# Optimization experiments

Measured on AMD Instinct MI355X. Metric: run time of the kernel, lower is better.

Reference implementation:

```python
import jax, jax.numpy as jnp
import numpy as np

C = 96
H = 4 * C  # hidden_channels = int(mlp_ratio * in_channels)
EPS = 1e-5  # torch LayerNorm default eps


def setup_inputs() -> dict:
    key = jax.random.key(0)
    ks = jax.random.split(key, 8)
    x = jax.random.normal(ks[0], (2, C, 64, 64, 64), dtype=jnp.float32)
    # depthwise conv3d: groups=C -> kernel (O=C, I/groups=1, 7,7,7)
    dw_w = jax.random.normal(ks[1], (C, 1, 7, 7, 7), dtype=jnp.float32) * 0.05
    dw_b = jax.random.normal(ks[2], (C,), dtype=jnp.float32) * 0.01
    ln_g = jnp.ones((C,), dtype=jnp.float32)
    ln_b = jnp.zeros((C,), dtype=jnp.float32)
    w1 = jax.random.normal(ks[3], (C, H), dtype=jnp.float32) * (1.0 / np.sqrt(C))
    b1 = jnp.zeros((H,), dtype=jnp.float32)
    w2 = jax.random.normal(ks[4], (H, C), dtype=jnp.float32) * (1.0 / np.sqrt(H))
    b2 = jnp.zeros((C,), dtype=jnp.float32)
    gamma = jnp.full((C,), 1e-6, dtype=jnp.float32)  # layer_scale init
    return {"x": x, "dw_w": dw_w, "dw_b": dw_b, "ln_g": ln_g, "ln_b": ln_b,
            "w1": w1, "b1": b1, "w2": w2, "b2": b2, "gamma": gamma}


def reference(x, dw_w, dw_b, ln_g, ln_b, w1, b1, w2, b2, gamma):
    # depthwise 3D conv, kernel 7, padding 3 (same), groups=C
    out = jax.lax.conv_general_dilated(
        x, dw_w, window_strides=(1, 1, 1), padding=[(3, 3)] * 3,
        dimension_numbers=("NCDHW", "OIDHW", "NCDHW"),
        feature_group_count=C)
    out = out + dw_b[None, :, None, None, None]
    # b c d h w -> b d h w c
    out = jnp.moveaxis(out, 1, -1)
    # LayerNorm over channel dim
    mu = jnp.mean(out, axis=-1, keepdims=True)
    var = jnp.mean(jnp.square(out - mu), axis=-1, keepdims=True)
    out = (out - mu) * jax.lax.rsqrt(var + EPS) * ln_g + ln_b
    # 2-layer MLP (pointwise convs as Linear), exact GELU like torch default
    out = jax.nn.gelu(out @ w1 + b1, approximate=False)
    out = out @ w2 + b2
    # layer scale
    out = gamma * out
    # b d h w c -> b c d h w, stochastic depth is identity (p=0), residual
    out = jnp.moveaxis(out, -1, 1)
    return out + x
```

## Files before the change

kernel.cpp:

```cpp
#include <hip/hip_runtime.h>

typedef unsigned int u32;
typedef unsigned short u16;
typedef unsigned long long u64;
typedef long i64;
typedef float f32x4 __attribute__((ext_vector_type(4)));
typedef float f32x2 __attribute__((ext_vector_type(2)));
typedef u32 u32x4 __attribute__((ext_vector_type(4)));

__device__ __forceinline__ u16 f2bf_rne(float f) {
    return __builtin_bit_cast(u16, (__bf16)f);
}
__device__ __forceinline__ float bf2f(u16 h) {
    return __builtin_bit_cast(float, ((u32)h) << 16);
}
__device__ __forceinline__ float gelu_fast(float v) {
    float t = __builtin_amdgcn_exp2f(v * -2.4554673f);
    return v * __builtin_amdgcn_rcpf(1.f + t);
}
__device__ __forceinline__ i64 mk64(u32 lo, u32 hi) {
    return (i64)(((u64)hi << 32) | (u64)lo);
}
__device__ __forceinline__ u32 pk4(float a, float b, float c, float d) {
    u32 w = (u32)__builtin_amdgcn_cvt_pk_fp8_f32(a, b, 0, false);
    return (u32)__builtin_amdgcn_cvt_pk_fp8_f32(c, d, (int)w, true);
}
__device__ __forceinline__ unsigned char f2fp8(float a) {
    u32 w = (u32)__builtin_amdgcn_cvt_pk_fp8_f32(a, 0.f, 0, false);
    return (unsigned char)(w & 0xffu);
}

__global__ void prep_weights(const float* __restrict__ w1, const float* __restrict__ w2,
                             const float* __restrict__ lng, const float* __restrict__ lnb,
                             const float* __restrict__ b1,
                             i64* __restrict__ W1L, i64* __restrict__ W2L,
                             float* __restrict__ B1s) {
    int i = blockIdx.x * 256 + threadIdx.x;
    if (i < 4608) {
        int n16 = i / 192, r = i - n16 * 192;
        int kk = r >> 6, lane = r & 63;
        int n = n16 * 16 + (lane & 15);
        int cb = kk * 32 + (lane >> 4) * 8;
        float s0 = lng[cb + 0] * w1[(cb + 0) * 384 + n];
        float s1 = lng[cb + 1] * w1[(cb + 1) * 384 + n];
        float s2 = lng[cb + 2] * w1[(cb + 2) * 384 + n];
        float s3 = lng[cb + 3] * w1[(cb + 3) * 384 + n];
        float s4 = lng[cb + 4] * w1[(cb + 4) * 384 + n];
        float s5 = lng[cb + 5] * w1[(cb + 5) * 384 + n];
        float s6 = lng[cb + 6] * w1[(cb + 6) * 384 + n];
        float s7 = lng[cb + 7] * w1[(cb + 7) * 384 + n];
        W1L[i] = mk64(pk4(s0, s1, s2, s3), pk4(s4, s5, s6, s7));
    } else if (i < 9216) {
        int e = i - 4608;
        int r = e & 767, lane = r & 63, jk = r >> 6;
        int c = ((e / 768) * 16) + (lane & 15);
        int nb = jk * 32 + (lane >> 4) * 8;
        float s0 = w2[(nb + 0) * 96 + c], s1 = w2[(nb + 1) * 96 + c];
        float s2 = w2[(nb + 2) * 96 + c], s3 = w2[(nb + 3) * 96 + c];
        float s4 = w2[(nb + 4) * 96 + c], s5 = w2[(nb + 5) * 96 + c];
        float s6 = w2[(nb + 6) * 96 + c], s7 = w2[(nb + 7) * 96 + c];
        W2L[e] = mk64(pk4(s0, s1, s2, s3), pk4(s4, s5, s6, s7));
    } else if (i < 9600) {
        int n = i - 9216;
        float s = b1[n];
        for (int c = 0; c < 96; ++c) s += lnb[c] * w1[c * 384 + n];
        B1s[n] = s;
    }
}

__global__ void prep_bt(const float* __restrict__ dww, unsigned char* __restrict__ BT) {
    int i = blockIdx.x * 256 + threadIdx.x;
    if (i >= 301056) return;
    int lane = i & 63;
    int tap = (i >> 6) % 49;
    int c = i / 3136;
    int n = lane & 15, kg = lane >> 4;
    const float* wt = dww + c * 343 + tap * 7;
    float e[8];
#pragma unroll
    for (int j = 0; j < 8; ++j) {
        int t = kg * 8 + j - n;
        e[j] = (t >= 0 && t < 7) ? wt[t] : 0.f;
    }
    u32 lo = pk4(e[0], e[1], e[2], e[3]);
    u32 hi = pk4(e[4], e[5], e[6], e[7]);
    *(u32*)&BT[(size_t)i * 8] = lo;
    *(u32*)&BT[(size_t)i * 8 + 4] = hi;
}

template<int PACKED>
__global__ __launch_bounds__(512, 8) void dwconvM(const float* __restrict__ x,
                                                  const unsigned char* __restrict__ BT,
                                                  const float* __restrict__ dwb,
                                                  unsigned char* __restrict__ cw8,
                                                  u16* __restrict__ o16) {
    __shared__ __align__(16) unsigned char tile[42592];
    const int tid = threadIdx.x;
    const int bx = blockIdx.x, c = blockIdx.y, b = blockIdx.z;
    const int d0 = (bx >> 2) * 16, h0 = (bx & 3) * 16;
    const float* xc = x + ((size_t)(b * 96 + c)) * 262144;

    for (int i = tid; i < 9680; i += 512) {
        int pz = i / 440;
        int rem = i - pz * 440;
        int row = rem / 20;
        int u = rem - row * 20;
        int d = d0 + pz - 3, h = h0 + row - 3;
        u32 pk = 0;
        if (((unsigned)d < 64u) && ((unsigned)h < 64u)) {
            const float* xr = xc + d * 4096 + h * 64;
            if (u >= 1 && u <= 15) {
                float e[4];
                __builtin_memcpy(e, xr + 4 * u - 3, 16);
                pk = pk4(e[0], e[1], e[2], e[3]);
            } else if (u == 0) {
                pk = pk4(0.f, 0.f, 0.f, xr[0]);
            } else if (u == 16) {
                pk = pk4(xr[61], xr[62], xr[63], 0.f);
            }
        }
        *(u32*)&tile[(pz * 22 + row) * 88 + u * 4] = pk;
    }
    __syncthreads();

    const int lane = tid & 63, wv = tid >> 6;
    const int n = lane & 15, g = lane >> 4;
    const unsigned char* BTl = BT + (size_t)c * 49 * 512 + (size_t)lane * 8;
    const int abase = n * 88 + 8 * g;
    const float bias = dwb[c];

#pragma unroll
    for (int plane = 0; plane < 2; ++plane) {
        const int dd = wv + plane * 8;

        f32x4 acc[4];
#pragma unroll
        for (int i = 0; i < 4; ++i) acc[i] = f32x4{0.f, 0.f, 0.f, 0.f};

        i64 bfC[7], bfN[7];
#pragma unroll
        for (int kh = 0; kh < 7; ++kh)
            bfC[kh] = *(const i64*)(BTl + (size_t)kh * 512);

#pragma unroll
        for (int kd = 0; kd < 7; ++kd) {
#pragma unroll
            for (int kh = 0; kh < 7; ++kh)
                bfN[kh] = (kd < 6) ? *(const i64*)(BTl + (size_t)((kd + 1) * 7 + kh) * 512)
                                   : (i64)0;
            const unsigned char* tb = &tile[(dd + kd) * 1936 + abase];
#pragma unroll
            for (int kh = 0; kh < 7; ++kh) {
                const unsigned char* ab = tb + kh * 88;
#pragma unroll
                for (int wt = 0; wt < 4; ++wt) {
                    i64 af = *(const i64*)(ab + 16 * wt);
                    acc[wt] = __builtin_amdgcn_mfma_f32_16x16x32_fp8_fp8(af, bfC[kh], acc[wt], 0, 0, 0);
                }
            }
#pragma unroll
            for (int kh = 0; kh < 7; ++kh) bfC[kh] = bfN[kh];
        }

        const int d = d0 + dd;
#pragma unroll
        for (int wt = 0; wt < 4; ++wt) {
#pragma unroll
            for (int q = 0; q < 4; ++q) {
                int h = h0 + 4 * g + q;
                int w = wt * 16 + n;
                size_t pos = (size_t)b * 262144 + (size_t)d * 4096 + h * 64 + w;
                if (PACKED == 0)
                    cw8[(size_t)c * 524288 + pos] = f2fp8(acc[wt][q] + bias);
                else
                    o16[2 * ((size_t)(b * 96 + c) * 262144 + (size_t)d * 4096 + h * 64 + w) + 1] =
                        f2bf_rne(acc[wt][q] + bias);
            }
        }
    }
}

template<int PACKED>
__global__ __launch_bounds__(256, 5) void dwconvA(const float* __restrict__ x,
                                                  const float* __restrict__ dww,
                                                  const float* __restrict__ dwb,
                                                  u32* cw, u16* o16) {
    __shared__ u32 tile32[7920];
    const int tid = threadIdx.x;
    const int bx = blockIdx.x, c = blockIdx.y, b = blockIdx.z;
    const int d0 = (bx >> 2) * 4, h0 = (bx & 3) * 16;
    const float* xc = x + ((size_t)(b * 96 + c)) * 262144;

    for (int i = tid; i < 7700; i += 256) {
        int pz = i / 770;
        int rem = i - pz * 770;
        int r2 = rem / 70;
        int col = rem - r2 * 70;
        int d = d0 + pz - 3, h = h0 + 2 * r2 - 3, w = col - 3;
        float lo = 0.f, hi = 0.f;
        if (((unsigned)d < 64u) && ((unsigned)w < 64u)) {
            int base = d * 4096 + h * 64 + w;
            if ((unsigned)h < 64u) lo = xc[base];
            if ((unsigned)(h + 1) < 64u) hi = xc[base + 64];
        }
        int a = pz * 792 + r2 * 72 + col;
        int aw = ((((a >> 2) ^ ((a >> 5) & 1)) << 2)) | (a & 3);
        tile32[aw] = (u32)f2bf_rne(lo) | ((u32)f2bf_rne(hi) << 16);
    }
    __syncthreads();

    const int tx = tid & 7, ty = (tid >> 3) & 7, tz = tid >> 6;
    float a0[8], a1[8];
#pragma unroll
    for (int i = 0; i < 8; ++i) { a0[i] = 0.f; a1[i] = 0.f; }

    for (int kd = 0; kd < 7; ++kd) {
        const float* Wk = dww + c * 343 + kd * 49;
        const int pz = tz + kd;
#pragma unroll
        for (int pr = 0; pr < 4; ++pr) {
            const int g0 = pz * 198 + (ty + pr) * 18 + (tx << 1);
            u32 rb[16];
#pragma unroll
            for (int k = 0; k < 4; ++k) {
                int g = g0 + k;
                int ga = (g ^ ((g >> 3) & 1)) << 2;
                *(u32x4*)&rb[4 * k] = *(const u32x4*)(tile32 + ga);
            }
            float rlo[16], rhi[16];
#pragma unroll
            for (int t = 0; t < 16; ++t) {
                rlo[t] = __builtin_bit_cast(float, rb[t] << 16);
                rhi[t] = __builtin_bit_cast(float, rb[t]);
            }
#pragma unroll
            for (int kw = 0; kw < 7; ++kw) {
                float wA = Wk[2 * pr * 7 + kw];
#pragma unroll
                for (int i = 0; i < 8; ++i) {
                    a0[i] = fmaf(rlo[kw + i], wA, a0[i]);
                    a1[i] = fmaf(rhi[kw + i], wA, a1[i]);
                }
                if (pr < 3) {
                    float wB = Wk[(2 * pr + 1) * 7 + kw];
#pragma unroll
                    for (int i = 0; i < 8; ++i) a0[i] = fmaf(rhi[kw + i], wB, a0[i]);
                }
                if (pr > 0) {
                    float wC = Wk[(2 * pr - 1) * 7 + kw];
#pragma unroll
                    for (int i = 0; i < 8; ++i) a1[i] = fmaf(rlo[kw + i], wC, a1[i]);
                }
            }
        }
    }

    const float bias = dwb[c];
    const int d = d0 + tz;
    const int hA = h0 + 2 * ty;
    {
        size_t e = ((size_t)(b * 96 + c)) * 262144 + d * 4096 + hA * 64 + 8 * tx;
#pragma unroll
        for (int i = 0; i < 8; ++i) o16[2 * (e + i) + 1] = f2bf_rne(a0[i] + bias);
#pragma unroll
        for (int i = 0; i < 8; ++i) o16[2 * (e + 64 + i) + 1] = f2bf_rne(a1[i] + bias);
    }
    (void)cw;
}

template<int CWP, int WF>
__global__ __launch_bounds__(256, 4) void mlp3(const void* cwsrc,
                                               const i64* __restrict__ W1L,
                                               const i64* __restrict__ W2L,
                                               const float* __restrict__ B1s,
                                               const float* __restrict__ w1f,
                                               const float* __restrict__ w2f,
                                               const float* __restrict__ lng,
                                               const float* __restrict__ lnb,
                                               const float* __restrict__ b1g,
                                               const float* __restrict__ b2g,
                                               const float* __restrict__ gam,
                                               const float* __restrict__ x,
                                               float* __restrict__ out) {
    __shared__ __align__(16) unsigned char HS[4][2][1152];

    const int tid = threadIdx.x;
    const int wv = tid >> 6, lane = tid & 63;
    const int p = lane & 15, G = lane >> 4;
    const int pos0 = blockIdx.x * 128 + wv * 32;
    const int b = pos0 >> 18, prel0 = pos0 & 262143;
    unsigned char* hsw = &HS[wv][0][0];

    float v0[3][8], v1[3][8];
    if (CWP == 0) {
        const u16* cwp = (const u16*)cwsrc;
#pragma unroll
        for (int kk = 0; kk < 3; ++kk)
#pragma unroll
            for (int m = 0; m < 8; ++m) {
                int c = kk * 32 + G * 8 + m;
                u16 w = cwp[(size_t)c * 262144 + (pos0 >> 1) + p];
                f32x2 pr = __builtin_amdgcn_cvt_pk_f32_fp8((int)(u32)w, false);
                v0[kk][m] = pr[0];
                v1[kk][m] = pr[1];
            }
    } else {
        const u32* ow = (const u32*)cwsrc;
#pragma unroll
        for (int kk = 0; kk < 3; ++kk)
#pragma unroll
            for (int m = 0; m < 8; ++m) {
                int c = kk * 32 + G * 8 + m;
                size_t base = ((size_t)(b * 96 + c)) * 262144 + prel0 + 2 * p;
                v0[kk][m] = bf2f((u16)(ow[base] >> 16));
                v1[kk][m] = bf2f((u16)(ow[base + 1] >> 16));
            }
    }

    float s0 = 0.f, sq0 = 0.f, s1 = 0.f, sq1 = 0.f;
#pragma unroll
    for (int kk = 0; kk < 3; ++kk)
#pragma unroll
        for (int m = 0; m < 8; ++m) {
            s0 += v0[kk][m]; sq0 += v0[kk][m] * v0[kk][m];
            s1 += v1[kk][m]; sq1 += v1[kk][m] * v1[kk][m];
        }
    s0 += __shfl_xor(s0, 16); sq0 += __shfl_xor(sq0, 16);
    s0 += __shfl_xor(s0, 32); sq0 += __shfl_xor(sq0, 32);
    s1 += __shfl_xor(s1, 16); sq1 += __shfl_xor(sq1, 16);
    s1 += __shfl_xor(s1, 32); sq1 += __shfl_xor(sq1, 32);
    float mu0 = s0 * (1.f / 96.f);
    float rstd0 = rsqrtf(sq0 * (1.f / 96.f) - mu0 * mu0 + 1e-5f);
    float mu1 = s1 * (1.f / 96.f);
    float rstd1 = rsqrtf(sq1 * (1.f / 96.f) - mu1 * mu1 + 1e-5f);

    i64 aF[2][3];
#pragma unroll
    for (int kk = 0; kk < 3; ++kk) {
        aF[0][kk] = mk64(
            pk4((v0[kk][0] - mu0) * rstd0, (v0[kk][1] - mu0) * rstd0,
                (v0[kk][2] - mu0) * rstd0, (v0[kk][3] - mu0) * rstd0),
            pk4((v0[kk][4] - mu0) * rstd0, (v0[kk][5] - mu0) * rstd0,
                (v0[kk][6] - mu0) * rstd0, (v0[kk][7] - mu0) * rstd0));
        aF[1][kk] = mk64(
            pk4((v1[kk][0] - mu1) * rstd1, (v1[kk][1] - mu1) * rstd1,
                (v1[kk][2] - mu1) * rstd1, (v1[kk][3] - mu1) * rstd1),
            pk4((v1[kk][4] - mu1) * rstd1, (v1[kk][5] - mu1) * rstd1,
                (v1[kk][6] - mu1) * rstd1, (v1[kk][7] - mu1) * rstd1));
    }

    f32x4 acc[2][6];
#pragma unroll
    for (int t = 0; t < 2; ++t)
#pragma unroll
        for (int i = 0; i < 6; ++i) acc[t][i] = f32x4{0.f, 0.f, 0.f, 0.f};

    for (int j = 0; j < 6; ++j) {
        i64 wf[12];
#pragma unroll
        for (int q = 0; q < 12; ++q) {
            if (WF == 0) {
                wf[q] = W1L[(j * 12 + q) * 64 + lane];
            } else {
                int nt = q / 3, kk = q - nt * 3;
                int nn = (j * 4 + nt) * 16 + p;
                int cb = kk * 32 + G * 8;
                wf[q] = mk64(
                    pk4(lng[cb + 0] * w1f[(cb + 0) * 384 + nn], lng[cb + 1] * w1f[(cb + 1) * 384 + nn],
                        lng[cb + 2] * w1f[(cb + 2) * 384 + nn], lng[cb + 3] * w1f[(cb + 3) * 384 + nn]),
                    pk4(lng[cb + 4] * w1f[(cb + 4) * 384 + nn], lng[cb + 5] * w1f[(cb + 5) * 384 + nn],
                        lng[cb + 6] * w1f[(cb + 6) * 384 + nn], lng[cb + 7] * w1f[(cb + 7) * 384 + nn]));
            }
        }
        f32x4 bb[4];
#pragma unroll
        for (int nt = 0; nt < 4; ++nt)
            bb[nt] = *(const f32x4*)&B1s[(j * 4 + nt) * 16 + 4 * G];

#pragma unroll
        for (int t = 0; t < 2; ++t) {
            f32x4 c1[4];
#pragma unroll
            for (int nt = 0; nt < 4; ++nt) {
                c1[nt] = f32x4{0.f, 0.f, 0.f, 0.f};
#pragma unroll
                for (int kk = 0; kk < 3; ++kk)
                    c1[nt] = __builtin_amdgcn_mfma_f32_16x16x32_fp8_fp8(wf[nt * 3 + kk], aF[t][kk], c1[nt], 0, 0, 0);
            }
#pragma unroll
            for (int nt = 0; nt < 4; ++nt) {
                float g0 = gelu_fast(c1[nt][0] + bb[nt][0]);
                float g1 = gelu_fast(c1[nt][1] + bb[nt][1]);
                float g2 = gelu_fast(c1[nt][2] + bb[nt][2]);
                float g3 = gelu_fast(c1[nt][3] + bb[nt][3]);
                *(u32*)&hsw[t * 1152 + p * 72 + nt * 16 + 4 * G] = pk4(g0, g1, g2, g3);
            }
        }

        i64 w2r[12];
#pragma unroll
        for (int q = 0; q < 12; ++q) {
            int ct = q >> 1, kkj = q & 1;
            if (WF == 0) {
                w2r[q] = W2L[(ct * 12 + j * 2 + kkj) * 64 + lane];
            } else {
                int cc = ct * 16 + p;
                int nb = (j * 2 + kkj) * 32 + G * 8;
                w2r[q] = mk64(
                    pk4(w2f[(nb + 0) * 96 + cc], w2f[(nb + 1) * 96 + cc],
                        w2f[(nb + 2) * 96 + cc], w2f[(nb + 3) * 96 + cc]),
                    pk4(w2f[(nb + 4) * 96 + cc], w2f[(nb + 5) * 96 + cc],
                        w2f[(nb + 6) * 96 + cc], w2f[(nb + 7) * 96 + cc]));
            }
        }

        asm volatile("s_waitcnt lgkmcnt(0)" ::: "memory");
        __builtin_amdgcn_sched_barrier(0);

        i64 hF[2][2];
#pragma unroll
        for (int t = 0; t < 2; ++t)
#pragma unroll
            for (int kkj = 0; kkj < 2; ++kkj)
                hF[t][kkj] = *(const i64*)&hsw[t * 1152 + p * 72 + kkj * 32 + G * 8];

#pragma unroll
        for (int ct = 0; ct < 6; ++ct)
#pragma unroll
            for (int kkj = 0; kkj < 2; ++kkj) {
#pragma unroll
                for (int t = 0; t < 2; ++t)
                    acc[t][ct] = __builtin_amdgcn_mfma_f32_16x16x32_fp8_fp8(hF[t][kkj], w2r[ct * 2 + kkj], acc[t][ct], 0, 0, 0);
            }
    }

#pragma unroll
    for (int ct = 0; ct < 6; ++ct) {
        int c = ct * 16 + p;
        float b2c = b2g[c], gc = gam[c];
#pragma unroll
        for (int k = 0; k < 2; ++k) {
            size_t xi = ((size_t)(b * 96 + c)) * 262144 + prel0 + 8 * G + 4 * k;
            f32x4 xv = *(const f32x4*)&x[xi];
            f32x4 o;
            o[0] = (acc[0][ct][2 * k]     + b2c) * gc + xv[0];
            o[1] = (acc[1][ct][2 * k]     + b2c) * gc + xv[1];
            o[2] = (acc[0][ct][2 * k + 1] + b2c) * gc + xv[2];
            o[3] = (acc[1][ct][2 * k + 1] + b2c) * gc + xv[3];
            *(f32x4*)&out[xi] = o;
        }
    }
}

extern "C" void kernel_launch(void* const* d_in, const int* in_sizes, int n_in,
                              void* d_out, int out_size, void* d_ws, size_t ws_size,
                              hipStream_t stream) {
    const float* x   = (const float*)d_in[0];
    const float* dww = (const float*)d_in[1];
    const float* dwb = (const float*)d_in[2];
    const float* lng = (const float*)d_in[3];
    const float* lnb = (const float*)d_in[4];
    const float* w1  = (const float*)d_in[5];
    const float* b1  = (const float*)d_in[6];
    const float* w2  = (const float*)d_in[7];
    const float* b2  = (const float*)d_in[8];
    const float* gam = (const float*)d_in[9];
    float* out = (float*)d_out;

    const size_t NEED_W  = 75264;
    const size_t NEED_BT = 75264 + 2408448ull;
    const size_t NEED_FULL = NEED_BT + 50331648ull;
    const bool wsW  = ws_size >= NEED_W;
    const bool wsBT = ws_size >= NEED_BT;
    const bool wsCW = ws_size >= NEED_FULL;

    i64* W1L = (i64*)d_ws;
    i64* W2L = (i64*)((char*)d_ws + 36864);
    float* B1s = (float*)((char*)d_ws + 73728);
    unsigned char* BT = (unsigned char*)d_ws + 75264;
    unsigned char* cw8 = (unsigned char*)d_ws + 2483712;

    if (wsW)
        hipLaunchKernelGGL(prep_weights, dim3(38), dim3(256), 0, stream,
                           w1, w2, lng, lnb, b1, W1L, W2L, B1s);
    if (wsBT)
        hipLaunchKernelGGL(prep_bt, dim3(1176), dim3(256), 0, stream, dww, BT);

    dim3 g1(16, 96, 2), blkc(512);
    if (wsCW)
        hipLaunchKernelGGL((dwconvM<0>), g1, blkc, 0, stream, x, BT, dwb, cw8, (u16*)d_out);
    else if (wsBT)
        hipLaunchKernelGGL((dwconvM<1>), g1, blkc, 0, stream, x, BT, dwb, cw8, (u16*)d_out);
    else {
        dim3 g1a(64, 96, 2), blka(256);
        hipLaunchKernelGGL((dwconvA<1>), g1a, blka, 0, stream, x, dww, dwb, (u32*)cw8, (u16*)d_out);
    }

    dim3 g2(4096), blk2(256);
    if (wsCW)
        hipLaunchKernelGGL((mlp3<0, 0>), g2, blk2, 0, stream, (const void*)cw8,
                           W1L, W2L, B1s, w1, w2, lng, lnb, b1, b2, gam, x, out);
    else if (wsW)
        hipLaunchKernelGGL((mlp3<1, 0>), g2, blk2, 0, stream, (const void*)d_out,
                           W1L, W2L, B1s, w1, w2, lng, lnb, b1, b2, gam, x, out);
    else
        hipLaunchKernelGGL((mlp3<1, 1>), g2, blk2, 0, stream, (const void*)d_out,
                           W1L, W2L, B1s, w1, w2, lng, lnb, b1, b2, gam, x, out);
}
```

Baseline: 372.0 us.

## Compute two adjacent depth planes per wave sharing A-fragment LDS loads

Each wave now computes two adjacent output depth planes (2*wv and 2*wv+1) together instead of two planes eight apart. One pass over eight input planes feeds both accumulators, so each A fragment read from LDS is used twice, with the current and previous kd weight fragments. This roughly halves LDS reads of the input tile per output and cuts repeated weight loads. In exchange the kernel holds twice the accumulators plus two weight register sets, so launch bounds drop from 8 to 4 waves-per-SIMD hint, which lowers occupancy.

Result: slower. 399.4 us (+7.4%).

```diff
diff --git a/kernel.cpp b/kernel.cpp
--- a/kernel.cpp
+++ b/kernel.cpp
@@ -89,7 +89,7 @@
 }
 
 template<int PACKED>
-__global__ __launch_bounds__(512, 8) void dwconvM(const float* __restrict__ x,
+__global__ __launch_bounds__(512, 4) void dwconvM(const float* __restrict__ x,
                                                   const unsigned char* __restrict__ BT,
                                                   const float* __restrict__ dwb,
                                                   unsigned char* __restrict__ cw8,
@@ -129,52 +129,54 @@
     const int abase = n * 88 + 8 * g;
     const float bias = dwb[c];
 
-#pragma unroll
-    for (int plane = 0; plane < 2; ++plane) {
-        const int dd = wv + plane * 8;
-
-        f32x4 acc[4];
-#pragma unroll
-        for (int i = 0; i < 4; ++i) acc[i] = f32x4{0.f, 0.f, 0.f, 0.f};
-
-        i64 bfC[7], bfN[7];
-#pragma unroll
-        for (int kh = 0; kh < 7; ++kh)
-            bfC[kh] = *(const i64*)(BTl + (size_t)kh * 512);
-
-#pragma unroll
-        for (int kd = 0; kd < 7; ++kd) {
+    f32x4 acc0[4], acc1[4];
+#pragma unroll
+    for (int i = 0; i < 4; ++i) {
+        acc0[i] = f32x4{0.f, 0.f, 0.f, 0.f};
+        acc1[i] = f32x4{0.f, 0.f, 0.f, 0.f};
+    }
+
+    i64 bfC[7], bfP[7];
+#pragma unroll
+    for (int ip = 0; ip < 8; ++ip) {
+        if (ip <= 6) {
 #pragma unroll
             for (int kh = 0; kh < 7; ++kh)
-                bfN[kh] = (kd < 6) ? *(const i64*)(BTl + (size_t)((kd + 1) * 7 + kh) * 512)
-                                   : (i64)0;
-            const unsigned char* tb = &tile[(dd + kd) * 1936 + abase];
-#pragma unroll
-            for (int kh = 0; kh < 7; ++kh) {
-                const unsigned char* ab = tb + kh * 88;
-#pragma unroll
-                for (int wt = 0; wt < 4; ++wt) {
-                    i64 af = *(const i64*)(ab + 16 * wt);
-                    acc[wt] = __builtin_amdgcn_mfma_f32_16x16x32_fp8_fp8(af, bfC[kh], acc[wt], 0, 0, 0);
-                }
-            }
-#pragma unroll
-            for (int kh = 0; kh < 7; ++kh) bfC[kh] = bfN[kh];
-        }
-
-        const int d = d0 + dd;
+                bfC[kh] = *(const i64*)(BTl + (size_t)(ip * 7 + kh) * 512);
+        }
+        const unsigned char* tb = &tile[(2 * wv + ip) * 1936 + abase];
+#pragma unroll
+        for (int kh = 0; kh < 7; ++kh) {
+            const unsigned char* ab = tb + kh * 88;
+#pragma unroll
+            for (int wt = 0; wt < 4; ++wt) {
+                i64 af = *(const i64*)(ab + 16 * wt);
+                if (ip <= 6)
+                    acc0[wt] = __builtin_amdgcn_mfma_f32_16x16x32_fp8_fp8(af, bfC[kh], acc0[wt], 0, 0, 0);
+                if (ip >= 1)
+                    acc1[wt] = __builtin_amdgcn_mfma_f32_16x16x32_fp8_fp8(af, bfP[kh], acc1[wt], 0, 0, 0);
+            }
+        }
+#pragma unroll
+        for (int kh = 0; kh < 7; ++kh) bfP[kh] = bfC[kh];
+    }
+
+#pragma unroll
+    for (int pl = 0; pl < 2; ++pl) {
+        const int d = d0 + 2 * wv + pl;
 #pragma unroll
         for (int wt = 0; wt < 4; ++wt) {
 #pragma unroll
             for (int q = 0; q < 4; ++q) {
                 int h = h0 + 4 * g + q;
                 int w = wt * 16 + n;
+                float val = (pl == 0 ? acc0[wt][q] : acc1[wt][q]) + bias;
                 size_t pos = (size_t)b * 262144 + (size_t)d * 4096 + h * 64 + w;
                 if (PACKED == 0)
-                    cw8[(size_t)c * 524288 + pos] = f2fp8(acc[wt][q] + bias);
+                    cw8[(size_t)c * 524288 + pos] = f2fp8(val);
                 else
                     o16[2 * ((size_t)(b * 96 + c) * 262144 + (size_t)d * 4096 + h * 64 + w) + 1] =
-                        f2bf_rne(acc[wt][q] + bias);
+                        f2bf_rne(val);
             }
         }
     }
```
